# Performance work log

Measured on AMD Instinct MI355X. Metric: run time of the kernel, lower is better.

Reference implementation:

```python
import jax, jax.numpy as jnp
import numpy as np

N_E = 4096
E_DIM = 64
BETA = 0.25


def setup_inputs() -> dict:
    key = jax.random.key(0)
    k1, k2 = jax.random.split(key)
    z = jax.random.normal(k1, (16, E_DIM, 32, 32), dtype=jnp.float32)
    embedding = jax.random.normal(k2, (N_E, E_DIM), dtype=jnp.float32)
    return {"z": z, "embedding": embedding}


def reference(z, embedding):
    # b c h w -> b h w c
    zc = jnp.transpose(z, (0, 2, 3, 1))  # [B,H,W,C]
    B, H, W, C = zc.shape
    zf = zc.reshape(-1, C)  # [N, C]

    # Squared Euclidean distances (argmin is identical to cdist p=2 argmin)
    # d2[n,e] = |z|^2 - 2 z.e + |e|^2
    d2 = (
        jnp.sum(zf * zf, axis=1, keepdims=True)
        - 2.0 * (zf @ embedding.T)
        + jnp.sum(embedding * embedding, axis=1)[None, :]
    )  # [N, n_e]
    idx = jnp.argmin(d2, axis=1)  # [N]

    z_q = embedding[idx].reshape(B, H, W, C)

    # dist_p == 2 losses
    loss_d1 = jnp.mean((jax.lax.stop_gradient(z_q) - zc) ** 2)
    loss_d2 = jnp.mean((z_q - jax.lax.stop_gradient(zc)) ** 2)
    loss = BETA * loss_d1 + loss_d2

    # Straight-through estimator
    z_q = zc + jax.lax.stop_gradient(z_q - zc)

    indices = idx.reshape(B, H, W)
    z_q = jnp.transpose(z_q, (0, 3, 1, 2))  # b h w c -> b c h w
    return z_q, loss, indices
```

## Files before the change

kernel.cpp:

```cpp
#include <hip/hip_runtime.h>

typedef float f32x4 __attribute__((ext_vector_type(4)));
typedef short bf16x8 __attribute__((ext_vector_type(8)));

#define HW_ 1024
#define NE_ 4096
#define CHW_ 65536
#define ZQ_SIZE 1048576
#define LOSS_OFF ZQ_SIZE
#define IDX_OFF (ZQ_SIZE + 1)
#define LOSS_SCALE (1.25f / 1048576.f)
#define EPS_GAP 0.1f

union FragU { unsigned u[4]; bf16x8 v; };

__device__ __forceinline__ unsigned umin_(unsigned a, unsigned b) { return a < b ? a : b; }
__device__ __forceinline__ unsigned umax_(unsigned a, unsigned b) { return a > b ? a : b; }

__device__ __forceinline__ void top2_(unsigned key, unsigned& s1, unsigned& s2) {
    unsigned t;
    asm("v_med3_u32 %0, %1, %2, %3" : "=v"(t) : "v"(key), "v"(s1), "v"(s2));
    s2 = t;
    s1 = umin_(s1, key);
}

__device__ __forceinline__ void split8(const float* v, FragU& hi, FragU& lo) {
#pragma unroll
    for (int p = 0; p < 4; p++) {
        float a = v[2 * p], b = v[2 * p + 1];
        unsigned ua = __float_as_uint(a), ub = __float_as_uint(b);
        hi.u[p] = (ua >> 16) | (ub & 0xFFFF0000u);
        float la = a - __uint_as_float(ua & 0xFFFF0000u);
        float lb = b - __uint_as_float(ub & 0xFFFF0000u);
        lo.u[p] = (__float_as_uint(la) >> 16) | (__float_as_uint(lb) & 0xFFFF0000u);
    }
}

__device__ __forceinline__ void gload_lds16(const void* g, void* l) {
    __builtin_amdgcn_global_load_lds(
        (const __attribute__((address_space(1))) unsigned*)g,
        (__attribute__((address_space(3))) unsigned*)l, 16, 0, 0);
}

__global__ __launch_bounds__(256) void vq_eprep(
        const float* __restrict__ emb, char* __restrict__ efrag,
        float* __restrict__ h_e, float* __restrict__ out) {
    const int bid = blockIdx.x, tid = threadIdx.x;
    if (bid < 128) {
        int u = bid * 256 + tid;
        int l = u & 63, s = (u >> 6) & 1, t = u >> 7;
        int er = t * 16 + (l & 15);
        int c0 = s * 32 + (l >> 4) * 8;
        const float* ep = emb + (size_t)er * 64 + c0;
        float4 ea = *(const float4*)(ep);
        float4 eb = *(const float4*)(ep + 4);
        float v[8];
        v[0] = -ea.x; v[1] = -ea.y; v[2] = -ea.z; v[3] = -ea.w;
        v[4] = -eb.x; v[5] = -eb.y; v[6] = -eb.z; v[7] = -eb.w;
        FragU hi, lo;
        split8(v, hi, lo);
        char* base = efrag + (size_t)t * 4096 + l * 16;
        *(FragU*)(base + s * 1024) = hi;
        *(FragU*)(base + (2 + s) * 1024) = lo;
    } else {
        int t = (bid - 128) * 256 + tid;
        const float4* er = (const float4*)(emb + (size_t)t * 64);
        float s = 0.f;
#pragma unroll
        for (int k = 0; k < 16; k++) {
            float4 e4 = er[k];
            s = fmaf(e4.x, e4.x, s); s = fmaf(e4.y, e4.y, s);
            s = fmaf(e4.z, e4.z, s); s = fmaf(e4.w, e4.w, s);
        }
        h_e[t] = 0.5f * s;
        if (t == 0) out[LOSS_OFF] = 0.f;
    }
}

__global__ __launch_bounds__(512) void vq_mfma(
        const float* __restrict__ z, const char* __restrict__ efrag,
        const float* __restrict__ h_e,
        unsigned* __restrict__ k1q, unsigned* __restrict__ k2q) {
    __shared__ char buf[2][32768];
    __shared__ __attribute__((aligned(16))) float sh_he[512];

    const int tid = threadIdx.x;
    const int lane = tid & 63;
    const int w = tid >> 6;
    const int lrow = lane & 15;
    const int lgrp = lane >> 4;
    const int es = blockIdx.x >> 5;
    const int rb = blockIdx.x & 31;
    const int e0t = es * 32;
    const int rt0 = rb * 32 + w * 4;
    const int b = rb >> 1;

    sh_he[tid] = h_e[es * 512 + tid];

    {
        const char* src = efrag + (size_t)(e0t + w) * 4096 + lane * 16;
        char* dst = buf[0] + w * 4096;
#pragma unroll
        for (int i = 0; i < 4; i++) gload_lds16(src + i * 1024, dst + i * 1024);
    }

    bf16x8 zh[4][2], zl[4][2];
    float hz[4];
#pragma unroll
    for (int r = 0; r < 4; r++) {
        float ss = 0.f;
#pragma unroll
        for (int s = 0; s < 2; s++) {
            const int hw = ((rt0 + r) * 16 + lrow) & 1023;
            const int c0 = s * 32 + lgrp * 8;
            const float* zp = z + (size_t)b * CHW_ + hw;
            float v[8];
#pragma unroll
            for (int j = 0; j < 8; j++) {
                v[j] = zp[(c0 + j) * HW_];
                ss = fmaf(v[j], v[j], ss);
            }
            FragU hi, lo;
            split8(v, hi, lo);
            zh[r][s] = hi.v;
            zl[r][s] = lo.v;
        }
        ss += __shfl_xor(ss, 16);
        ss += __shfl_xor(ss, 32);
        hz[r] = 0.5f * ss;
    }

    unsigned s1k[4] = {~0u, ~0u, ~0u, ~0u};
    unsigned s2k[4] = {~0u, ~0u, ~0u, ~0u};

#define MFMA_STEP(JJ, A0, A1, A2, A3)                                          \
    do {                                                                       \
        const char* tb = cb + (JJ) * 4096;                                     \
        bf16x8 ah0 = *(const bf16x8*)(tb);                                     \
        bf16x8 ah1 = *(const bf16x8*)(tb + 1024);                              \
        bf16x8 al0 = *(const bf16x8*)(tb + 2048);                              \
        bf16x8 al1 = *(const bf16x8*)(tb + 3072);                              \
        const f32x4 he = *(const f32x4*)&sh_he[(c * 8 + (JJ)) * 16 + lgrp * 4];\
        A0 = he + hz[0]; A1 = he + hz[1]; A2 = he + hz[2]; A3 = he + hz[3];    \
        __builtin_amdgcn_s_setprio(1);                                         \
        A0 = __builtin_amdgcn_mfma_f32_16x16x32_bf16(ah0, zh[0][0], A0, 0, 0, 0); \
        A1 = __builtin_amdgcn_mfma_f32_16x16x32_bf16(ah0, zh[1][0], A1, 0, 0, 0); \
        A2 = __builtin_amdgcn_mfma_f32_16x16x32_bf16(ah0, zh[2][0], A2, 0, 0, 0); \
        A3 = __builtin_amdgcn_mfma_f32_16x16x32_bf16(ah0, zh[3][0], A3, 0, 0, 0); \
        A0 = __builtin_amdgcn_mfma_f32_16x16x32_bf16(ah1, zh[0][1], A0, 0, 0, 0); \
        A1 = __builtin_amdgcn_mfma_f32_16x16x32_bf16(ah1, zh[1][1], A1, 0, 0, 0); \
        A2 = __builtin_amdgcn_mfma_f32_16x16x32_bf16(ah1, zh[2][1], A2, 0, 0, 0); \
        A3 = __builtin_amdgcn_mfma_f32_16x16x32_bf16(ah1, zh[3][1], A3, 0, 0, 0); \
        A0 = __builtin_amdgcn_mfma_f32_16x16x32_bf16(al0, zh[0][0], A0, 0, 0, 0); \
        A1 = __builtin_amdgcn_mfma_f32_16x16x32_bf16(al0, zh[1][0], A1, 0, 0, 0); \
        A2 = __builtin_amdgcn_mfma_f32_16x16x32_bf16(al0, zh[2][0], A2, 0, 0, 0); \
        A3 = __builtin_amdgcn_mfma_f32_16x16x32_bf16(al0, zh[3][0], A3, 0, 0, 0); \
        A0 = __builtin_amdgcn_mfma_f32_16x16x32_bf16(al1, zh[0][1], A0, 0, 0, 0); \
        A1 = __builtin_amdgcn_mfma_f32_16x16x32_bf16(al1, zh[1][1], A1, 0, 0, 0); \
        A2 = __builtin_amdgcn_mfma_f32_16x16x32_bf16(al1, zh[2][1], A2, 0, 0, 0); \
        A3 = __builtin_amdgcn_mfma_f32_16x16x32_bf16(al1, zh[3][1], A3, 0, 0, 0); \
        A0 = __builtin_amdgcn_mfma_f32_16x16x32_bf16(ah0, zl[0][0], A0, 0, 0, 0); \
        A1 = __builtin_amdgcn_mfma_f32_16x16x32_bf16(ah0, zl[1][0], A1, 0, 0, 0); \
        A2 = __builtin_amdgcn_mfma_f32_16x16x32_bf16(ah0, zl[2][0], A2, 0, 0, 0); \
        A3 = __builtin_amdgcn_mfma_f32_16x16x32_bf16(ah0, zl[3][0], A3, 0, 0, 0); \
        A0 = __builtin_amdgcn_mfma_f32_16x16x32_bf16(ah1, zl[0][1], A0, 0, 0, 0); \
        A1 = __builtin_amdgcn_mfma_f32_16x16x32_bf16(ah1, zl[1][1], A1, 0, 0, 0); \
        A2 = __builtin_amdgcn_mfma_f32_16x16x32_bf16(ah1, zl[2][1], A2, 0, 0, 0); \
        A3 = __builtin_amdgcn_mfma_f32_16x16x32_bf16(ah1, zl[3][1], A3, 0, 0, 0); \
        __builtin_amdgcn_s_setprio(0);                                         \
    } while (0)

#define KEY4(EB, A0, A1, A2, A3)                                               \
    do {                                                                       \
        _Pragma("unroll")                                                      \
        for (int rr = 0; rr < 4; rr++) {                                       \
            top2_((__float_as_uint((A0)[rr]) & 0xFFFFF000u) | ((EB) + rr), s1k[0], s2k[0]); \
            top2_((__float_as_uint((A1)[rr]) & 0xFFFFF000u) | ((EB) + rr), s1k[1], s2k[1]); \
            top2_((__float_as_uint((A2)[rr]) & 0xFFFFF000u) | ((EB) + rr), s1k[2], s2k[2]); \
            top2_((__float_as_uint((A3)[rr]) & 0xFFFFF000u) | ((EB) + rr), s1k[3], s2k[3]); \
        }                                                                      \
    } while (0)

    __syncthreads();
    for (int c = 0; c < 4; c++) {
        if (c < 3) {
            const char* src = efrag + (size_t)(e0t + (c + 1) * 8 + w) * 4096
                              + lane * 16;
            char* dst = buf[(c + 1) & 1] + w * 4096;
#pragma unroll
            for (int i = 0; i < 4; i++) gload_lds16(src + i * 1024, dst + i * 1024);
        }

        const char* cb = buf[c & 1] + lane * 16;

        f32x4 p0, p1, p2, p3;
        MFMA_STEP(0, p0, p1, p2, p3);
        unsigned peb = (unsigned)(es * 512 + (c * 8) * 16 + lgrp * 4);
#pragma unroll
        for (int j = 1; j < 8; j++) {
            f32x4 q0, q1, q2, q3;
            MFMA_STEP(j, q0, q1, q2, q3);
            KEY4(peb, p0, p1, p2, p3);
            p0 = q0; p1 = q1; p2 = q2; p3 = q3;
            peb = (unsigned)(es * 512 + (c * 8 + j) * 16 + lgrp * 4);
        }
        KEY4(peb, p0, p1, p2, p3);

        __syncthreads();
    }
#undef MFMA_STEP
#undef KEY4

#pragma unroll
    for (int off = 16; off <= 32; off += 16) {
#pragma unroll
        for (int r = 0; r < 4; r++) {
            unsigned o1 = (unsigned)__shfl_xor((int)s1k[r], off);
            unsigned o2 = (unsigned)__shfl_xor((int)s2k[r], off);
            s2k[r] = umin_(umin_(s2k[r], o2), umax_(s1k[r], o1));
            s1k[r] = umin_(s1k[r], o1);
        }
    }

    if (lane < 16) {
        const int base = es * 16384;
#pragma unroll
        for (int r = 0; r < 4; r++) {
            k1q[base + (rt0 + r) * 16 + lane] = s1k[r];
            k2q[base + (rt0 + r) * 16 + lane] = s2k[r];
        }
    }
}

__global__ __launch_bounds__(256) void vq_final(
        const float* __restrict__ z, const float* __restrict__ emb,
        const unsigned* __restrict__ k1q, const unsigned* __restrict__ k2q,
        float* __restrict__ out) {
    int t = blockIdx.x * 256 + threadIdx.x;
    int n = t & 16383;
    int q = t >> 14;

    unsigned m = 0xFFFFFFFFu, s = 0xFFFFFFFFu;
#pragma unroll
    for (int i = 0; i < 8; i++) {
        unsigned a = k1q[i * 16384 + n];
        unsigned b = k2q[i * 16384 + n];
        unsigned hi = umax_(m, a);
        m = umin_(m, a);
        s = umin_(umin_(s, b), hi);
    }

    int idx = (int)(m & 0xFFFu);
    float s1 = __uint_as_float(m & 0xFFFFF000u);
    float s2 = __uint_as_float(s & 0xFFFFF000u);

    int b = n >> 10, hw = n & 1023;
    const float* zp = z + (size_t)b * CHW_ + hw;
    const int cq = q * 16;

    if (s2 - s1 < EPS_GAP) {
        int i2 = (int)(s & 0xFFFu);
        const float* ea = emb + (size_t)idx * 64;
        const float* eb = emb + (size_t)i2 * 64;
        double da = 0.0, db = 0.0;
#pragma unroll 8
        for (int c = 0; c < 64; c++) {
            double zv = (double)zp[c * HW_];
            double xa = (double)ea[c] - zv;
            double xb = (double)eb[c] - zv;
            da = fma(xa, xa, da);
            db = fma(xb, xb, db);
        }
        if (db < da || (db == da && i2 < idx)) idx = i2;
    }

    const float* er = emb + (size_t)idx * 64 + cq;
    float* zq = out + (size_t)b * CHW_ + hw;
    float lsum = 0.f;
#pragma unroll
    for (int j = 0; j < 16; j++) {
        float e = er[j];
        float d = e - zp[(cq + j) * HW_];
        zq[(cq + j) * HW_] = e;
        lsum = fmaf(d, d, lsum);
    }
    if (q == 0) out[IDX_OFF + n] = (float)idx;

#pragma unroll
    for (int off = 32; off; off >>= 1) lsum += __shfl_down(lsum, off);
    if ((threadIdx.x & 63) == 0) atomicAdd(&out[LOSS_OFF], lsum * LOSS_SCALE);
}

extern "C" void kernel_launch(void* const* d_in, const int* in_sizes, int n_in,
                              void* d_out, int out_size, void* d_ws, size_t ws_size,
                              hipStream_t stream) {
    const float* z   = (const float*)d_in[0];
    const float* emb = (const float*)d_in[1];
    float* out = (float*)d_out;
    char* ws = (char*)d_ws;

    char* efrag   = ws;
    float* h_e    = (float*)(ws + 1048576);
    unsigned* k1q = (unsigned*)(ws + 1065024);
    unsigned* k2q = (unsigned*)(ws + 1589312);

    vq_eprep<<<144, 256, 0, stream>>>(emb, efrag, h_e, out);
    vq_mfma <<<256, 512, 0, stream>>>(z, efrag, h_e, k1q, k2q);
    vq_final<<<256, 256, 0, stream>>>(z, emb, k1q, k2q, out);
}
```

Baseline: 51.57 us.

## Fuse embedding prep into MFMA kernel, building bf16 split fragments in LDS

Removes the separate embedding-prep kernel. Each MFMA block now computes its own half-norms of the codebook rows and splits them into hi/lo bf16 fragments, writing them straight into LDS instead of copying pre-built fragments from workspace. This saves one kernel launch and the workspace round trip. The cost is redundant prep work: each embedding chunk is rebuilt by all 32 row-blocks, and the next chunk's build is now synchronous register work rather than an async global-to-LDS load. It also drops the s_setprio hints around the MFMA sequence and zeroes the loss slot with a memset instead.

```diff
diff --git a/kernel.cpp b/kernel.cpp
--- a/kernel.cpp
+++ b/kernel.cpp
@@ -36,50 +36,8 @@
     }
 }
 
-__device__ __forceinline__ void gload_lds16(const void* g, void* l) {
-    __builtin_amdgcn_global_load_lds(
-        (const __attribute__((address_space(1))) unsigned*)g,
-        (__attribute__((address_space(3))) unsigned*)l, 16, 0, 0);
-}
-
-__global__ __launch_bounds__(256) void vq_eprep(
-        const float* __restrict__ emb, char* __restrict__ efrag,
-        float* __restrict__ h_e, float* __restrict__ out) {
-    const int bid = blockIdx.x, tid = threadIdx.x;
-    if (bid < 128) {
-        int u = bid * 256 + tid;
-        int l = u & 63, s = (u >> 6) & 1, t = u >> 7;
-        int er = t * 16 + (l & 15);
-        int c0 = s * 32 + (l >> 4) * 8;
-        const float* ep = emb + (size_t)er * 64 + c0;
-        float4 ea = *(const float4*)(ep);
-        float4 eb = *(const float4*)(ep + 4);
-        float v[8];
-        v[0] = -ea.x; v[1] = -ea.y; v[2] = -ea.z; v[3] = -ea.w;
-        v[4] = -eb.x; v[5] = -eb.y; v[6] = -eb.z; v[7] = -eb.w;
-        FragU hi, lo;
-        split8(v, hi, lo);
-        char* base = efrag + (size_t)t * 4096 + l * 16;
-        *(FragU*)(base + s * 1024) = hi;
-        *(FragU*)(base + (2 + s) * 1024) = lo;
-    } else {
-        int t = (bid - 128) * 256 + tid;
-        const float4* er = (const float4*)(emb + (size_t)t * 64);
-        float s = 0.f;
-#pragma unroll
-        for (int k = 0; k < 16; k++) {
-            float4 e4 = er[k];
-            s = fmaf(e4.x, e4.x, s); s = fmaf(e4.y, e4.y, s);
-            s = fmaf(e4.z, e4.z, s); s = fmaf(e4.w, e4.w, s);
-        }
-        h_e[t] = 0.5f * s;
-        if (t == 0) out[LOSS_OFF] = 0.f;
-    }
-}
-
 __global__ __launch_bounds__(512) void vq_mfma(
-        const float* __restrict__ z, const char* __restrict__ efrag,
-        const float* __restrict__ h_e,
+        const float* __restrict__ z, const float* __restrict__ emb,
         unsigned* __restrict__ k1q, unsigned* __restrict__ k2q) {
     __shared__ char buf[2][32768];
     __shared__ __attribute__((aligned(16))) float sh_he[512];
@@ -95,14 +53,43 @@
     const int rt0 = rb * 32 + w * 4;
     const int b = rb >> 1;
 
-    sh_he[tid] = h_e[es * 512 + tid];
-
     {
-        const char* src = efrag + (size_t)(e0t + w) * 4096 + lane * 16;
-        char* dst = buf[0] + w * 4096;
-#pragma unroll
-        for (int i = 0; i < 4; i++) gload_lds16(src + i * 1024, dst + i * 1024);
-    }
+        const float4* er = (const float4*)(emb + (size_t)(es * 512 + tid) * 64);
+        float s = 0.f;
+#pragma unroll
+        for (int k = 0; k < 16; k++) {
+            float4 e4 = er[k];
+            s = fmaf(e4.x, e4.x, s); s = fmaf(e4.y, e4.y, s);
+            s = fmaf(e4.z, e4.z, s); s = fmaf(e4.w, e4.w, s);
+        }
+        sh_he[tid] = 0.5f * s;
+    }
+
+#define BUILD_CHUNK(CC, DST)                                                   \
+    do {                                                                       \
+        const int tt = tid >> 6, l = tid & 63;                                 \
+        const int erow = (e0t + (CC) * 8 + tt) * 16 + (l & 15);                \
+        const float* ep = emb + (size_t)erow * 64 + (l >> 4) * 8;              \
+        float4 a0 = *(const float4*)(ep);                                      \
+        float4 b0 = *(const float4*)(ep + 4);                                  \
+        float4 a1 = *(const float4*)(ep + 32);                                 \
+        float4 b1 = *(const float4*)(ep + 36);                                 \
+        float v0[8], v1[8];                                                    \
+        v0[0] = -a0.x; v0[1] = -a0.y; v0[2] = -a0.z; v0[3] = -a0.w;            \
+        v0[4] = -b0.x; v0[5] = -b0.y; v0[6] = -b0.z; v0[7] = -b0.w;            \
+        v1[0] = -a1.x; v1[1] = -a1.y; v1[2] = -a1.z; v1[3] = -a1.w;            \
+        v1[4] = -b1.x; v1[5] = -b1.y; v1[6] = -b1.z; v1[7] = -b1.w;            \
+        FragU h0, l0, h1, l1;                                                  \
+        split8(v0, h0, l0);                                                    \
+        split8(v1, h1, l1);                                                    \
+        char* base_ = (DST) + tt * 4096 + l * 16;                              \
+        *(FragU*)(base_)        = h0;                                          \
+        *(FragU*)(base_ + 1024) = h1;                                          \
+        *(FragU*)(base_ + 2048) = l0;                                          \
+        *(FragU*)(base_ + 3072) = l1;                                          \
+    } while (0)
+
+    BUILD_CHUNK(0, buf[0]);
 
     bf16x8 zh[4][2], zl[4][2];
     float hz[4];
@@ -142,7 +129,6 @@
         bf16x8 al1 = *(const bf16x8*)(tb + 3072);                              \
         const f32x4 he = *(const f32x4*)&sh_he[(c * 8 + (JJ)) * 16 + lgrp * 4];\
         A0 = he + hz[0]; A1 = he + hz[1]; A2 = he + hz[2]; A3 = he + hz[3];    \
-        __builtin_amdgcn_s_setprio(1);                                         \
         A0 = __builtin_amdgcn_mfma_f32_16x16x32_bf16(ah0, zh[0][0], A0, 0, 0, 0); \
         A1 = __builtin_amdgcn_mfma_f32_16x16x32_bf16(ah0, zh[1][0], A1, 0, 0, 0); \
         A2 = __builtin_amdgcn_mfma_f32_16x16x32_bf16(ah0, zh[2][0], A2, 0, 0, 0); \
@@ -167,7 +153,6 @@
         A1 = __builtin_amdgcn_mfma_f32_16x16x32_bf16(ah1, zl[1][1], A1, 0, 0, 0); \
         A2 = __builtin_amdgcn_mfma_f32_16x16x32_bf16(ah1, zl[2][1], A2, 0, 0, 0); \
         A3 = __builtin_amdgcn_mfma_f32_16x16x32_bf16(ah1, zl[3][1], A3, 0, 0, 0); \
-        __builtin_amdgcn_s_setprio(0);                                         \
     } while (0)
 
 #define KEY4(EB, A0, A1, A2, A3)                                               \
@@ -183,13 +168,8 @@
 
     __syncthreads();
     for (int c = 0; c < 4; c++) {
-        if (c < 3) {
-            const char* src = efrag + (size_t)(e0t + (c + 1) * 8 + w) * 4096
-                              + lane * 16;
-            char* dst = buf[(c + 1) & 1] + w * 4096;
-#pragma unroll
-            for (int i = 0; i < 4; i++) gload_lds16(src + i * 1024, dst + i * 1024);
-        }
+        if (c < 3)
+            BUILD_CHUNK(c + 1, buf[(c + 1) & 1]);
 
         const char* cb = buf[c & 1] + lane * 16;
 
@@ -210,6 +190,7 @@
     }
 #undef MFMA_STEP
 #undef KEY4
+#undef BUILD_CHUNK
 
 #pragma unroll
     for (int off = 16; off <= 32; off += 16) {
@@ -299,12 +280,10 @@
     float* out = (float*)d_out;
     char* ws = (char*)d_ws;
 
-    char* efrag   = ws;
-    float* h_e    = (float*)(ws + 1048576);
-    unsigned* k1q = (unsigned*)(ws + 1065024);
-    unsigned* k2q = (unsigned*)(ws + 1589312);
-
-    vq_eprep<<<144, 256, 0, stream>>>(emb, efrag, h_e, out);
-    vq_mfma <<<256, 512, 0, stream>>>(z, efrag, h_e, k1q, k2q);
+    unsigned* k1q = (unsigned*)ws;
+    unsigned* k2q = (unsigned*)(ws + 524288);
+
+    hipMemsetAsync(out + LOSS_OFF, 0, 4, stream);
+    vq_mfma <<<256, 512, 0, stream>>>(z, emb, k1q, k2q);
     vq_final<<<256, 256, 0, stream>>>(z, emb, k1q, k2q, out);
 }
```

New measurement: 56.54 us. 9.6% more time.
